# Kernel optimization log

Hardware: AMD Instinct MI355X
Metric: run time of the kernel (lower is better)

## Reference

```python
import jax, jax.numpy as jnp
import numpy as np

B, T, H, N = 2, 1024, 32, 64
HN = H * N              # 2048 hidden size
KVH, KVD = 8, 512       # GQA kv heads / kv width; repeat = HN // KVD = 4
LW, LA, LV, LG, LK = 64, 64, 32, 128, 32   # wavgk_split_list
EPS = 1e-6

def _rms(x, w):
    xf = x.astype(jnp.float32)
    var = jnp.mean(xf * xf, axis=-1, keepdims=True)
    return (w * (xf * jax.lax.rsqrt(var + EPS))).astype(x.dtype)

def _rot_half(x):
    x1, x2 = jnp.split(x, 2, axis=-1)
    return jnp.concatenate([-x2, x1], axis=-1)

def setup_inputs():
    key = jax.random.key(0)
    ks = iter(jax.random.split(key, 32))
    nrm = lambda s, sc=1.0: jax.random.normal(next(ks), s, jnp.float32) * sc
    d = {
        'x_in': nrm((B, T, HN)),
        'v_first': nrm((B, T, KVH, N)),
        'k_first': nrm((B, T, KVH, N)),
        'state': jnp.zeros((B, H, N, N), jnp.float32),
    }
    pos = jnp.arange(T, dtype=jnp.float32)
    inv = 1.0 / (10000.0 ** (jnp.arange(0, N, 2, dtype=jnp.float32) / N))
    ang = pos[:, None] * inv[None, :]
    ang = jnp.concatenate([ang, ang], axis=-1)   # [T, N]
    d['calc_cos'] = jnp.broadcast_to(jnp.cos(ang), (B, T, N))
    d['calc_sin'] = jnp.broadcast_to(jnp.sin(ang), (B, T, N))
    d.update(
        wavgk1=nrm((HN, LW + LA + LV + LG + LK), 0.02),
        w0=jnp.zeros((HN,), jnp.float32), w2=nrm((LW, HN), 0.02),
        a0=jnp.zeros((HN,), jnp.float32), a2=nrm((LA, HN), 0.02),
        v0=jnp.zeros((KVD,), jnp.float32), v2=nrm((LV, KVD), 0.02),
        g2=nrm((LG, HN), 0.02),
        k0=jnp.zeros((KVD,), jnp.float32), k2=nrm((LK, KVD), 0.02),
        r_k=nrm((H, N), 0.1),
        RKV_w=nrm((HN + 2 * KVD, HN), 0.02),
        O_w=nrm((HN, HN), 0.02),
        R_bias=jnp.zeros((HN,), jnp.float32),
        K_bias=jnp.zeros((KVD,), jnp.float32),
        V_bias=jnp.zeros((KVD,), jnp.float32),
        O_bias=jnp.zeros((HN,), jnp.float32),
        ln_r=jnp.ones((N,), jnp.float32),
        ln_k=jnp.ones((N,), jnp.float32),
        ln1=jnp.ones((HN,), jnp.float32),
    )
    return d

def reference(x_in, v_first, k_first, state, calc_cos, calc_sin, wavgk1, w0, w2,
              a0, a2, v0, v2, g2, k0, k2, r_k, RKV_w, O_w, R_bias, K_bias,
              V_bias, O_bias, ln_r, ln_k, ln1):
    rep = HN // KVD
    x = _rms(x_in, ln1)
    rkv = x @ RKV_w.T                                   # dense form of fpx_matmul
    r, k, v = jnp.split(rkv, [HN, HN + KVD], axis=-1)
    xw, xa, xv, xg, xk = jnp.split(x @ wavgk1, [LW, LW + LA, LW + LA + LV, LW + LA + LV + LG], axis=-1)
    r = r + R_bias; k = k + K_bias; v = v + V_bias
    r = _rms(r.reshape(B, T, H, N), ln_r)
    k = _rms(k.reshape(B, T, KVH, N), ln_k)
    cos, sin = calc_cos[:, :, None, :], calc_sin[:, :, None, :]   # unsqueeze_dim=2
    r = r * cos + _rot_half(r) * sin
    k = k * cos + _rot_half(k) * sin
    v = v.reshape(B, T, KVH, N)
    # layer_id > 0 path: gated residual toward layer-0 v/k
    gate_v = jax.nn.sigmoid(xv @ v2 + v0).reshape(B, T, KVH, N)
    v = v + (v_first - v) * gate_v
    gate_k = jax.nn.sigmoid(xk @ k2 + k0).reshape(B, T, KVH, N)
    k = k + (k_first - k) * gate_k
    w = jnp.tanh(xw) @ w2 + w0
    w = -jax.nn.softplus(-w) - 0.5
    # GQA repeat kv heads to H
    k = jnp.broadcast_to(k[:, :, :, None, :], (B, T, KVH, rep, N)).reshape(B, T, HN)
    v = jnp.broadcast_to(v[:, :, :, None, :], (B, T, KVH, rep, N)).reshape(B, T, HN)
    r = r.reshape(B, T, HN)
    a = jax.nn.sigmoid(xa @ a2 + a0)
    g = jax.nn.sigmoid(xg) @ g2
    kh = k.reshape(B, T, H, N)
    kk = (kh / jnp.maximum(jnp.linalg.norm(kh, axis=-1, keepdims=True), 1e-12)).reshape(B, T, HN)
    k = k * (1.0 - w + a)
    aa, bb = -kk, kk * a
    w = -jnp.exp(w.astype(jnp.float32))                 # log-decay (negative)
    # RWKV-7 recurrence: S <- S*diag(exp(w)) + (S a) b^T + v k^T ; o = S r
    hv = lambda t: jnp.moveaxis(t.reshape(B, T, H, N).astype(jnp.float32), 1, 0)
    def step(S, ts):
        r_t, w_t, k_t, v_t, a_t, b_t = ts               # each [B,H,N]
        sa = jnp.einsum('bhvk,bhk->bhv', S, a_t)
        S = S * jnp.exp(w_t)[:, :, None, :] + sa[..., None] * b_t[:, :, None, :] + v_t[..., None] * k_t[:, :, None, :]
        return S, jnp.einsum('bhvk,bhk->bhv', S, r_t)
    _, o = jax.lax.scan(step, state.astype(jnp.float32), (hv(r), hv(w), hv(k), hv(v), hv(aa), hv(bb)))
    xx = jnp.moveaxis(o, 0, 1).reshape(B, T, HN) * float(N) ** -0.5
    r_, k_, v_ = (t.reshape(B, T, H, N) for t in (r, k, v))
    bonus = (jnp.sum(r_ * k_ * r_k, axis=-1, keepdims=True) * v_).reshape(B, T, HN)
    xx = xx.astype(x_in.dtype) + bonus
    return x_in + (xx * g) @ O_w.T + O_bias
```

## Files before the change

### kernel.cpp

```cpp
#include <hip/hip_runtime.h>
#include <hip/hip_bf16.h>

#define B_ 2
#define T_ 1024
#define H_ 32
#define N_ 64
#define HN_ 2048
#define KVH_ 8
#define KVD_ 512
#define MTOK 2048
#define SMN 7168
#define KCAT 320
#define CH 64
#define NCH 16
#define NCHUNK 1024

typedef __bf16 bf16x8 __attribute__((ext_vector_type(8)));
typedef float f32x4 __attribute__((ext_vector_type(4)));
typedef float f32x2 __attribute__((ext_vector_type(2)));

__device__ __forceinline__ float sigmf(float x) { return 1.f / (1.f + expf(-x)); }

__global__ void f2b_kernel(const float* __restrict__ in, __hip_bfloat16* __restrict__ out, int n) {
    int i = blockIdx.x * 256 + threadIdx.x;
    if (i < n) out[i] = __float2bfloat16(in[i]);
}

__global__ void transpose_f2b_kernel(const float* __restrict__ in, __hip_bfloat16* __restrict__ out,
                                     int rows, int cols) {
    long i = (long)blockIdx.x * 256 + threadIdx.x;
    if (i >= (long)rows * cols) return;
    int c = (int)(i / rows), r = (int)(i % rows);
    out[i] = __float2bfloat16(in[(size_t)r * cols + c]);
}

__global__ void build_wcat_kernel(const float* __restrict__ w2, const float* __restrict__ a2,
                                  const float* __restrict__ v2, const float* __restrict__ g2,
                                  const float* __restrict__ k2, __hip_bfloat16* __restrict__ out) {
    long i = (long)blockIdx.x * 256 + threadIdx.x;
    if (i >= (long)SMN * KCAT) return;
    int j = (int)(i / KCAT), k = (int)(i % KCAT);
    float v = 0.f;
    if (j < 2048)      { if (k < 64)             v = w2[(size_t)k * 2048 + j]; }
    else if (j < 4096) { if (k >= 64 && k < 128)  v = a2[(size_t)(k - 64) * 2048 + (j - 2048)]; }
    else if (j < 4608) { if (k >= 128 && k < 160) v = v2[(size_t)(k - 128) * 512 + (j - 4096)]; }
    else if (j < 6656) { if (k >= 160 && k < 288) v = g2[(size_t)(k - 160) * 2048 + (j - 4608)]; }
    else               { if (k >= 288)            v = k2[(size_t)(k - 288) * 512 + (j - 6656)]; }
    out[i] = __float2bfloat16(v);
}

__global__ __launch_bounds__(256) void rmsnorm_kernel(const float* __restrict__ x,
                                                      const float* __restrict__ ln1,
                                                      __hip_bfloat16* __restrict__ out) {
    const int bt = blockIdx.x, tid = threadIdx.x;
    const float* row = x + (size_t)bt * HN_;
    float4 v0 = *(const float4*)(row + tid * 8);
    float4 v1 = *(const float4*)(row + tid * 8 + 4);
    float s = v0.x*v0.x + v0.y*v0.y + v0.z*v0.z + v0.w*v0.w
            + v1.x*v1.x + v1.y*v1.y + v1.z*v1.z + v1.w*v1.w;
    for (int m = 1; m < 64; m <<= 1) s += __shfl_xor(s, m);
    __shared__ float red[4];
    if ((tid & 63) == 0) red[tid >> 6] = s;
    __syncthreads();
    s = red[0] + red[1] + red[2] + red[3];
    float scale = rsqrtf(s * (1.f / HN_) + 1e-6f);
    float vals[8] = {v0.x, v0.y, v0.z, v0.w, v1.x, v1.y, v1.z, v1.w};
    #pragma unroll
    for (int j = 0; j < 8; ++j)
        out[(size_t)bt * HN_ + tid * 8 + j] = __float2bfloat16(vals[j] * scale * ln1[tid * 8 + j]);
}

__global__ void xwmod_kernel(const float* __restrict__ in, __hip_bfloat16* __restrict__ out) {
    long i = (long)blockIdx.x * 256 + threadIdx.x;
    if (i >= (long)MTOK * KCAT) return;
    int c = (int)(i % KCAT);
    float x = in[i];
    if (c < 64) x = tanhf(x);
    else if (c >= 160 && c < 288) x = sigmf(x);
    out[i] = __float2bfloat16(x);
}

__global__ __launch_bounds__(256) void gemm_bt(const __hip_bfloat16* __restrict__ A,
                                               const __hip_bfloat16* __restrict__ B,
                                               float* __restrict__ C, int M, int N, int K,
                                               const float* __restrict__ bias,
                                               const float* __restrict__ addend) {
    __shared__ __align__(16) __hip_bfloat16 As[64][40];
    __shared__ __align__(16) __hip_bfloat16 Bs[64][40];
    const int tid = threadIdx.x;
    const int wave = tid >> 6, lane = tid & 63;
    const int wr = (wave >> 1) * 32, wc = (wave & 1) * 32;
    const int brow = blockIdx.y << 6, bcol = blockIdx.x << 6;
    const int lrow = tid >> 2, lcol = (tid & 3) << 3;
    const int fr = lane & 15, ko = (lane >> 4) << 3;
    f32x4 acc[2][2] = {};
    for (int k0 = 0; k0 < K; k0 += 32) {
        uint4 av = *(const uint4*)(A + (size_t)(brow + lrow) * K + k0 + lcol);
        uint4 bv = *(const uint4*)(B + (size_t)(bcol + lrow) * K + k0 + lcol);
        *(uint4*)(&As[lrow][lcol]) = av;
        *(uint4*)(&Bs[lrow][lcol]) = bv;
        __syncthreads();
        bf16x8 af0 = *(const bf16x8*)(&As[wr + fr][ko]);
        bf16x8 af1 = *(const bf16x8*)(&As[wr + 16 + fr][ko]);
        bf16x8 bf0 = *(const bf16x8*)(&Bs[wc + fr][ko]);
        bf16x8 bf1 = *(const bf16x8*)(&Bs[wc + 16 + fr][ko]);
        acc[0][0] = __builtin_amdgcn_mfma_f32_16x16x32_bf16(af0, bf0, acc[0][0], 0, 0, 0);
        acc[0][1] = __builtin_amdgcn_mfma_f32_16x16x32_bf16(af0, bf1, acc[0][1], 0, 0, 0);
        acc[1][0] = __builtin_amdgcn_mfma_f32_16x16x32_bf16(af1, bf0, acc[1][0], 0, 0, 0);
        acc[1][1] = __builtin_amdgcn_mfma_f32_16x16x32_bf16(af1, bf1, acc[1][1], 0, 0, 0);
        __syncthreads();
    }
    const int cr = (lane >> 4) << 2, cc = lane & 15;
    #pragma unroll
    for (int i = 0; i < 2; ++i)
        #pragma unroll
        for (int j = 0; j < 2; ++j)
            #pragma unroll
            for (int r = 0; r < 4; ++r) {
                int row = brow + wr + i * 16 + cr + r;
                int col = bcol + wc + j * 16 + cc;
                float v = acc[i][j][r];
                if (bias) v += bias[col];
                if (addend) v += addend[(size_t)row * N + col];
                C[(size_t)row * N + col] = v;
            }
}

__global__ __launch_bounds__(256) void compose_kernel(
    const float* __restrict__ RKV, const float* __restrict__ SM,
    const float* __restrict__ v_first, const float* __restrict__ k_first,
    const float* __restrict__ cosd, const float* __restrict__ sind,
    const float* __restrict__ R_bias, const float* __restrict__ K_bias,
    const float* __restrict__ V_bias, const float* __restrict__ w0,
    const float* __restrict__ a0, const float* __restrict__ v0b,
    const float* __restrict__ k0b, const float* __restrict__ ln_r,
    const float* __restrict__ ln_k, const float* __restrict__ r_k,
    char* __restrict__ SC, __hip_bfloat16* __restrict__ VB, float* __restrict__ SB) {
    __shared__ __align__(16) float rbuf[HN_];
    __shared__ __align__(16) float kbuf[KVD_];
    __shared__ __align__(16) float vbuf[KVD_];
    __shared__ float knorms[KVH_];
    __shared__ float cosb[64], sinb[64];
    const int bt = blockIdx.x;
    const int b = bt >> 10, t = bt & 1023;
    const int tid = threadIdx.x;
    const float* rkvrow = RKV + (size_t)bt * 3072;
    const float* smrow = SM + (size_t)bt * SMN;

    if (tid < 64) {
        cosb[tid] = cosd[(size_t)bt * 64 + tid];
        sinb[tid] = sind[(size_t)bt * 64 + tid];
    }

    const int h = tid >> 3;
    const int off = (tid & 7) << 3;
    const int n0 = tid << 3;
    float rraw[8];
    {
        float4 x0 = *(const float4*)(rkvrow + n0);
        float4 x1 = *(const float4*)(rkvrow + n0 + 4);
        float4 b0 = *(const float4*)(R_bias + n0);
        float4 b1 = *(const float4*)(R_bias + n0 + 4);
        rraw[0] = x0.x + b0.x; rraw[1] = x0.y + b0.y; rraw[2] = x0.z + b0.z; rraw[3] = x0.w + b0.w;
        rraw[4] = x1.x + b1.x; rraw[5] = x1.y + b1.y; rraw[6] = x1.z + b1.z; rraw[7] = x1.w + b1.w;
    }
    float rss = 0.f;
    #pragma unroll
    for (int j = 0; j < 8; ++j) { rss += rraw[j] * rraw[j]; rbuf[n0 + j] = rraw[j]; }
    rss += __shfl_xor(rss, 1); rss += __shfl_xor(rss, 2); rss += __shfl_xor(rss, 4);
    float rscale = rsqrtf(rss * (1.f / 64.f) + 1e-6f);

    const int kvh = tid >> 5;
    const int ko2 = (tid & 31) << 1;
    const int kidx = kvh * 64 + ko2;
    float kraw0 = rkvrow[2048 + kidx] + K_bias[kidx];
    float kraw1 = rkvrow[2048 + kidx + 1] + K_bias[kidx + 1];
    float kss = kraw0 * kraw0 + kraw1 * kraw1;
    kss += __shfl_xor(kss, 1); kss += __shfl_xor(kss, 2); kss += __shfl_xor(kss, 4);
    kss += __shfl_xor(kss, 8); kss += __shfl_xor(kss, 16);
    float kscale = rsqrtf(kss * (1.f / 64.f) + 1e-6f);
    kbuf[kidx] = kraw0; kbuf[kidx + 1] = kraw1;

    {
        float va = rkvrow[2560 + kidx] + V_bias[kidx];
        float vb2 = rkvrow[2560 + kidx + 1] + V_bias[kidx + 1];
        float gv0 = sigmf(smrow[4096 + kidx] + v0b[kidx]);
        float gv1 = sigmf(smrow[4096 + kidx + 1] + v0b[kidx + 1]);
        vbuf[kidx] = va + (v_first[(size_t)bt * 512 + kidx] - va) * gv0;
        vbuf[kidx + 1] = vb2 + (v_first[(size_t)bt * 512 + kidx + 1] - vb2) * gv1;
    }
    __syncthreads();

    float rf[8];
    #pragma unroll
    for (int j = 0; j < 8; ++j) {
        int nn = off + j;
        int nn2 = (nn + 32) & 63;
        float val = rbuf[h * 64 + nn] * rscale * ln_r[nn];
        float oth = rbuf[h * 64 + nn2] * rscale * ln_r[nn2];
        float rot = (nn < 32) ? -oth : oth;
        rf[j] = val * cosb[nn] + rot * sinb[nn];
    }
    float kfv[2];
    #pragma unroll
    for (int j = 0; j < 2; ++j) {
        int nn = ko2 + j;
        int nn2 = (nn + 32) & 63;
        float val = kbuf[kvh * 64 + nn] * kscale * ln_k[nn];
        float oth = kbuf[kvh * 64 + nn2] * kscale * ln_k[nn2];
        float rot = (nn < 32) ? -oth : oth;
        float kr = val * cosb[nn] + rot * sinb[nn];
        float gk = sigmf(smrow[6656 + kvh * 64 + nn] + k0b[kvh * 64 + nn]);
        kfv[j] = kr + (k_first[(size_t)bt * 512 + kvh * 64 + nn] - kr) * gk;
    }
    __syncthreads();
    kbuf[kidx] = kfv[0]; kbuf[kidx + 1] = kfv[1];
    float kn = kfv[0] * kfv[0] + kfv[1] * kfv[1];
    kn += __shfl_xor(kn, 1); kn += __shfl_xor(kn, 2); kn += __shfl_xor(kn, 4);
    kn += __shfl_xor(kn, 8); kn += __shfl_xor(kn, 16);
    if ((tid & 31) == 0) knorms[kvh] = fmaxf(sqrtf(kn), 1e-12f);
    __syncthreads();

    const float knv = knorms[h >> 2];
    char* scb = SC + ((size_t)(b * H_ + h) * T_ + t) * 896;
    __hip_bfloat16* us = (__hip_bfloat16*)scb;
    float* df = (float*)(scb + 640);
    float4 w1a = *(const float4*)(smrow + n0);
    float4 w1b = *(const float4*)(smrow + n0 + 4);
    float4 ara = *(const float4*)(smrow + 2048 + n0);
    float4 arb = *(const float4*)(smrow + 2048 + n0 + 4);
    float w1arr[8] = {w1a.x, w1a.y, w1a.z, w1a.w, w1b.x, w1b.y, w1b.z, w1b.w};
    float aarr[8] = {ara.x, ara.y, ara.z, ara.w, arb.x, arb.y, arb.z, arb.w};
    float bsum = 0.f;
    #pragma unroll
    for (int j = 0; j < 8; ++j) {
        int nn = off + j, n = n0 + j;
        float w1 = w1arr[j] + w0[n];
        float w2v = -log1pf(expf(-w1)) - 0.5f;
        float av = sigmf(aarr[j] + a0[n]);
        float dec = expf(-expf(w2v));
        float kb = kbuf[(h >> 2) * 64 + nn];
        float vbv = vbuf[(h >> 2) * 64 + nn];
        float kkv = kb / knv;
        float ksc = kb * (1.f - w2v + av);
        us[nn]       = __float2bfloat16(rf[j]);
        us[64 + nn]  = __float2bfloat16(ksc);
        us[128 + nn] = __float2bfloat16(-kkv);
        us[192 + nn] = __float2bfloat16(kkv * av);
        us[256 + nn] = __float2bfloat16(vbv);
        df[nn] = dec;
        VB[(size_t)bt * HN_ + n] = __float2bfloat16(vbv);
        bsum += rf[j] * ksc * r_k[h * 64 + nn];
    }
    bsum += __shfl_xor(bsum, 1); bsum += __shfl_xor(bsum, 2); bsum += __shfl_xor(bsum, 4);
    if ((tid & 7) == 0) SB[bt * H_ + h] = bsum;
}

__global__ __launch_bounds__(64, 2) void scan_pass1(
    const char* __restrict__ SC, float* __restrict__ Q, float* __restrict__ O,
    float* __restrict__ Pf, float* __restrict__ Sf) {
    const int chunk = blockIdx.x;
    const int bh = chunk >> 4, c = chunk & 15;
    const int b = bh >> 5, h = bh & 31;
    const int lane = threadIdx.x;
    const char* base = SC + ((size_t)bh * T_ + (size_t)c * CH) * 896;

    f32x4 P4[16], S4[16];
    #pragma unroll
    for (int j = 0; j < 16; ++j) {
        #pragma unroll
        for (int e = 0; e < 4; ++e) {
            P4[j][e] = (4 * j + e == lane) ? 1.f : 0.f;
            S4[j][e] = 0.f;
        }
    }
    __shared__ __align__(16) float ld[2][5][64];
    float pr_r, pr_k, pr_a, pr_b, pr_v, pr_d;
    auto LOADT = [&](int t) {
        const __hip_bfloat16* us = (const __hip_bfloat16*)(base + (size_t)t * 896);
        pr_r = __bfloat162float(us[lane]);
        pr_k = __bfloat162float(us[64 + lane]);
        pr_a = __bfloat162float(us[128 + lane]);
        pr_b = __bfloat162float(us[192 + lane]);
        pr_v = __bfloat162float(us[256 + lane]);
        pr_d = *(const float*)(base + (size_t)t * 896 + 640 + 4 * lane);
    };
    LOADT(0);
    float* qbase = Q + (size_t)chunk * CH * 64 + lane;
    float* obase = O + ((size_t)b * T_ + (size_t)c * CH) * HN_ + h * 64 + lane;
    for (int t = 0; t < CH; ++t) {
        const int buf = t & 1;
        const float vt = pr_v;
        ld[buf][0][lane] = pr_a;
        ld[buf][1][lane] = pr_b;
        ld[buf][2][lane] = pr_d;
        ld[buf][3][lane] = pr_k;
        ld[buf][4][lane] = pr_r;
        __syncthreads();
        if (t + 1 < CH) LOADT(t + 1);
        f32x4 cp4 = {0,0,0,0}, sa4 = {0,0,0,0};
        #pragma unroll
        for (int j = 0; j < 16; ++j) {
            f32x4 a4 = *(const f32x4*)&ld[buf][0][4 * j];
            cp4 += P4[j] * a4;
            sa4 += S4[j] * a4;
        }
        const float cP = cp4[0] + cp4[1] + cp4[2] + cp4[3];
        const float sa = sa4[0] + sa4[1] + sa4[2] + sa4[3];
        const f32x4 cPv = {cP, cP, cP, cP}, sav = {sa, sa, sa, sa}, vtv = {vt, vt, vt, vt};
        f32x4 q4 = {0,0,0,0}, ol4 = {0,0,0,0};
        #pragma unroll
        for (int j = 0; j < 16; ++j) {
            f32x4 d4 = *(const f32x4*)&ld[buf][2][4 * j];
            f32x4 b4 = *(const f32x4*)&ld[buf][1][4 * j];
            f32x4 k4 = *(const f32x4*)&ld[buf][3][4 * j];
            f32x4 r4 = *(const f32x4*)&ld[buf][4][4 * j];
            f32x4 Pn = P4[j] * d4 + cPv * b4;
            f32x4 Sn = S4[j] * d4 + sav * b4 + vtv * k4;
            P4[j] = Pn; S4[j] = Sn;
            q4 += Pn * r4;
            ol4 += Sn * r4;
        }
        qbase[(size_t)t * 64] = q4[0] + q4[1] + q4[2] + q4[3];
        obase[(size_t)t * HN_] = ol4[0] + ol4[1] + ol4[2] + ol4[3];
        __syncthreads();
    }
    float* pf = Pf + (size_t)chunk * 4096 + lane * 64;
    float* sf = Sf + (size_t)chunk * 4096 + lane * 64;
    #pragma unroll
    for (int j = 0; j < 16; ++j) {
        *(f32x4*)(pf + 4 * j) = P4[j];
        *(f32x4*)(sf + 4 * j) = S4[j];
    }
}

__global__ __launch_bounds__(256) void scan_pass2(
    const float* __restrict__ Pf, float* __restrict__ Sf, const float* __restrict__ state) {
    const int blk = blockIdx.x;
    const int bh = blk >> 2, rb = blk & 3;
    const int tid = threadIdx.x;
    const int lv = tid >> 4, c0 = (tid & 15) << 2;
    __shared__ __align__(16) float S[16][68];
    __shared__ __align__(16) float P[64][64];

    *(f32x4*)&S[lv][c0] = *(const f32x4*)&state[(size_t)bh * 4096 + 1024 * rb + tid * 4];
    const size_t pbase = (size_t)(bh * NCH) * 4096;
    {
        f32x4 p0[4];
        #pragma unroll
        for (int j = 0; j < 4; ++j) p0[j] = *(const f32x4*)&Pf[pbase + tid * 16 + 4 * j];
        #pragma unroll
        for (int j = 0; j < 4; ++j) *(f32x4*)(&P[0][0] + tid * 16 + 4 * j) = p0[j];
    }
    __syncthreads();

    for (int c = 0; c < NCH; ++c) {
        const size_t ck = (size_t)(bh * NCH + c) * 4096;
        f32x4 pp[4];
        if (c + 1 < NCH) {
            #pragma unroll
            for (int j = 0; j < 4; ++j) pp[j] = *(const f32x4*)&Pf[ck + 4096 + tid * 16 + 4 * j];
        }
        f32x4 acc = *(const f32x4*)&Sf[ck + 1024 * rb + tid * 4];
        f32x4 cur = *(const f32x4*)&S[lv][c0];
        #pragma unroll 4
        for (int k4 = 0; k4 < 64; k4 += 4) {
            f32x4 sk4 = *(const f32x4*)&S[lv][k4];
            #pragma unroll
            for (int kk = 0; kk < 4; ++kk) {
                f32x4 pr = *(const f32x4*)&P[k4 + kk][c0];
                f32x4 sv = {sk4[kk], sk4[kk], sk4[kk], sk4[kk]};
                acc += sv * pr;
            }
        }
        __syncthreads();
        *(f32x4*)&S[lv][c0] = acc;
        if (c + 1 < NCH) {
            #pragma unroll
            for (int j = 0; j < 4; ++j) *(f32x4*)(&P[0][0] + tid * 16 + 4 * j) = pp[j];
        }
        *(f32x4*)&Sf[ck + 1024 * rb + tid * 4] = cur;
        __syncthreads();
    }
}

__global__ __launch_bounds__(64) void scan_pass3(
    const float* __restrict__ Q, const float* __restrict__ Sinit, float* __restrict__ O) {
    const int chunk = blockIdx.x;
    const int bh = chunk >> 4, c = chunk & 15;
    const int b = bh >> 5, h = bh & 31;
    const int t = threadIdx.x;
    __shared__ __align__(16) float S[64][64];
    #pragma unroll
    for (int j = 0; j < 16; ++j)
        *(f32x4*)&S[t][4 * j] = *(const f32x4*)&Sinit[(size_t)chunk * 4096 + (size_t)t * 64 + 4 * j];
    __syncthreads();
    float q[64];
    #pragma unroll
    for (int j = 0; j < 16; ++j)
        *(f32x4*)&q[4 * j] = *(const f32x4*)&Q[((size_t)chunk * CH + t) * 64 + 4 * j];
    float* orow = O + ((size_t)b * T_ + (size_t)c * CH + t) * HN_ + h * 64;
    #pragma unroll 4
    for (int v = 0; v < 64; ++v) {
        f32x4 a = {0, 0, 0, 0};
        #pragma unroll
        for (int j = 0; j < 16; ++j)
            a += *(const f32x4*)&S[v][4 * j] * *(const f32x4*)&q[4 * j];
        orow[v] = (a[0] + a[1] + a[2] + a[3] + orow[v]) * 0.125f;
    }
}

__global__ void post_kernel(const float* __restrict__ O, const float* __restrict__ SB,
                            const __hip_bfloat16* __restrict__ VB, const float* __restrict__ SM,
                            __hip_bfloat16* __restrict__ Ub) {
    long i = (long)blockIdx.x * 256 + threadIdx.x;
    if (i >= (long)MTOK * HN_) return;
    int bt = (int)(i >> 11), n = (int)(i & 2047), h = n >> 6;
    float u = (O[i] + SB[bt * H_ + h] * __bfloat162float(VB[i])) * SM[(size_t)bt * SMN + 4608 + n];
    Ub[i] = __float2bfloat16(u);
}

extern "C" void kernel_launch(void* const* d_in, const int* in_sizes, int n_in,
                              void* d_out, int out_size, void* d_ws, size_t ws_size,
                              hipStream_t stream) {
    (void)in_sizes; (void)n_in; (void)out_size; (void)ws_size;
    const float* x_in    = (const float*)d_in[0];
    const float* v_first = (const float*)d_in[1];
    const float* k_first = (const float*)d_in[2];
    const float* state   = (const float*)d_in[3];
    const float* calc_cos= (const float*)d_in[4];
    const float* calc_sin= (const float*)d_in[5];
    const float* wavgk1  = (const float*)d_in[6];
    const float* w0      = (const float*)d_in[7];
    const float* w2      = (const float*)d_in[8];
    const float* a0      = (const float*)d_in[9];
    const float* a2      = (const float*)d_in[10];
    const float* v0      = (const float*)d_in[11];
    const float* v2      = (const float*)d_in[12];
    const float* g2      = (const float*)d_in[13];
    const float* k0      = (const float*)d_in[14];
    const float* k2      = (const float*)d_in[15];
    const float* r_k     = (const float*)d_in[16];
    const float* RKV_w   = (const float*)d_in[17];
    const float* O_w     = (const float*)d_in[18];
    const float* R_bias  = (const float*)d_in[19];
    const float* K_bias  = (const float*)d_in[20];
    const float* V_bias  = (const float*)d_in[21];
    const float* O_bias  = (const float*)d_in[22];
    const float* ln_r    = (const float*)d_in[23];
    const float* ln_k    = (const float*)d_in[24];
    const float* ln1     = (const float*)d_in[25];
    float* out = (float*)d_out;

    char* ws = (char*)d_ws;
    size_t off = 0;
    auto alloc = [&](size_t bytes) -> char* {
        char* p = ws + off;
        off = (off + bytes + 255) & ~(size_t)255;
        return p;
    };
    float* SMf = (float*)alloc((size_t)MTOK * SMN * 4);
    char*  SCb = alloc((size_t)64 * T_ * 896);
    __hip_bfloat16* Ub = (__hip_bfloat16*)SCb;
    __hip_bfloat16* VBb = (__hip_bfloat16*)alloc((size_t)MTOK * HN_ * 2);
    float* SBf = (float*)alloc((size_t)MTOK * H_ * 4);
    float* Of  = (float*)alloc((size_t)MTOK * HN_ * 4);
    __hip_bfloat16* OWb = (__hip_bfloat16*)alloc((size_t)2048 * 2048 * 2);

    size_t ovl = off;
    __hip_bfloat16* Xb     = (__hip_bfloat16*)alloc((size_t)MTOK * HN_ * 2);
    __hip_bfloat16* RKVb   = (__hip_bfloat16*)alloc((size_t)3072 * 2048 * 2);
    __hip_bfloat16* WT1b   = (__hip_bfloat16*)alloc((size_t)320 * 2048 * 2);
    __hip_bfloat16* Wcatb  = (__hip_bfloat16*)alloc((size_t)SMN * KCAT * 2);
    __hip_bfloat16* XWmodb = (__hip_bfloat16*)alloc((size_t)MTOK * KCAT * 2);
    float* RKVf  = (float*)alloc((size_t)MTOK * 3072 * 4);
    float* XWraw = (float*)alloc((size_t)MTOK * KCAT * 4);
    off = ovl;
    float* Qf  = (float*)alloc((size_t)NCHUNK * CH * 64 * 4);
    float* Pff = (float*)alloc((size_t)NCHUNK * 4096 * 4);
    float* Sff = (float*)alloc((size_t)NCHUNK * 4096 * 4);

    f2b_kernel<<<(3072 * 2048 + 255) / 256, 256, 0, stream>>>(RKV_w, RKVb, 3072 * 2048);
    f2b_kernel<<<(2048 * 2048 + 255) / 256, 256, 0, stream>>>(O_w, OWb, 2048 * 2048);
    transpose_f2b_kernel<<<(320 * 2048 + 255) / 256, 256, 0, stream>>>(wavgk1, WT1b, 2048, 320);
    build_wcat_kernel<<<(SMN * KCAT + 255) / 256, 256, 0, stream>>>(w2, a2, v2, g2, k2, Wcatb);

    rmsnorm_kernel<<<MTOK, 256, 0, stream>>>(x_in, ln1, Xb);

    gemm_bt<<<dim3(3072 / 64, MTOK / 64), 256, 0, stream>>>(Xb, RKVb, RKVf, MTOK, 3072, 2048, nullptr, nullptr);
    gemm_bt<<<dim3(320 / 64, MTOK / 64), 256, 0, stream>>>(Xb, WT1b, XWraw, MTOK, 320, 2048, nullptr, nullptr);
    xwmod_kernel<<<(MTOK * KCAT + 255) / 256, 256, 0, stream>>>(XWraw, XWmodb);
    gemm_bt<<<dim3(SMN / 64, MTOK / 64), 256, 0, stream>>>(XWmodb, Wcatb, SMf, MTOK, SMN, KCAT, nullptr, nullptr);

    compose_kernel<<<MTOK, 256, 0, stream>>>(RKVf, SMf, v_first, k_first, calc_cos, calc_sin,
                                             R_bias, K_bias, V_bias, w0, a0, v0, k0,
                                             ln_r, ln_k, r_k, SCb, VBb, SBf);

    scan_pass1<<<NCHUNK, 64, 0, stream>>>(SCb, Qf, Of, Pff, Sff);
    scan_pass2<<<B_ * H_ * 4, 256, 0, stream>>>(Pff, Sff, state);
    scan_pass3<<<NCHUNK, 64, 0, stream>>>(Qf, Sff, Of);

    post_kernel<<<(MTOK * HN_ + 255) / 256, 256, 0, stream>>>(Of, SBf, VBb, SMf, Ub);
    gemm_bt<<<dim3(HN_ / 64, MTOK / 64), 256, 0, stream>>>(Ub, OWb, out, MTOK, HN_, 2048, O_bias, x_in);
}
```

Measured before the change: 452.9 us.

## Add 128x128 MFMA GEMM tile and split scan pass1 across two waves

Adds a 128x128-tile bf16 MFMA GEMM, with a 64x64 tile per wave, and uses it for the RKV, SM and output projections. This raises data reuse per global load and cuts the number of blocks. Separately, scan_pass1 now runs two waves per chunk: one wave evolves the P matrix and writes Q, the other evolves S and writes O. This halves the per-thread register state and serial work. The larger GEMM tiles lower occupancy and leave fewer blocks to fill the CUs, for example 24x16 blocks on the RKV GEMM.

After: 462.4 us. 2.1% more time.

```diff
diff --git a/kernel.cpp b/kernel.cpp
--- a/kernel.cpp
+++ b/kernel.cpp
@@ -124,6 +124,63 @@
                 if (addend) v += addend[(size_t)row * N + col];
                 C[(size_t)row * N + col] = v;
             }
+}
+
+__global__ __launch_bounds__(256) void gemm_bt128(const __hip_bfloat16* __restrict__ A,
+                                                  const __hip_bfloat16* __restrict__ B,
+                                                  float* __restrict__ C, int M, int N, int K,
+                                                  const float* __restrict__ bias,
+                                                  const float* __restrict__ addend) {
+    __shared__ __align__(16) __hip_bfloat16 As[128][40];
+    __shared__ __align__(16) __hip_bfloat16 Bs[128][40];
+    const int tid = threadIdx.x;
+    const int wave = tid >> 6, lane = tid & 63;
+    const int wr = (wave >> 1) * 64, wc = (wave & 1) * 64;
+    const int brow = blockIdx.y << 7, bcol = blockIdx.x << 7;
+    const int lrow = tid >> 2, lcol = (tid & 3) << 3;
+    const int fr = lane & 15, ko = (lane >> 4) << 3;
+    f32x4 acc[4][4] = {};
+    const __hip_bfloat16* Ap = A + (size_t)(brow + lrow) * K + lcol;
+    const __hip_bfloat16* Bp = B + (size_t)(bcol + lrow) * K + lcol;
+    const size_t half = (size_t)64 * K;
+    for (int k0 = 0; k0 < K; k0 += 32) {
+        uint4 a0 = *(const uint4*)(Ap + k0);
+        uint4 a1 = *(const uint4*)(Ap + half + k0);
+        uint4 b0 = *(const uint4*)(Bp + k0);
+        uint4 b1 = *(const uint4*)(Bp + half + k0);
+        *(uint4*)(&As[lrow][lcol]) = a0;
+        *(uint4*)(&As[lrow + 64][lcol]) = a1;
+        *(uint4*)(&Bs[lrow][lcol]) = b0;
+        *(uint4*)(&Bs[lrow + 64][lcol]) = b1;
+        __syncthreads();
+        bf16x8 af[4], bfr[4];
+        #pragma unroll
+        for (int i = 0; i < 4; ++i) {
+            af[i]  = *(const bf16x8*)(&As[wr + i * 16 + fr][ko]);
+            bfr[i] = *(const bf16x8*)(&Bs[wc + i * 16 + fr][ko]);
+        }
+        #pragma unroll
+        for (int i = 0; i < 4; ++i)
+            #pragma unroll
+            for (int j = 0; j < 4; ++j)
+                acc[i][j] = __builtin_amdgcn_mfma_f32_16x16x32_bf16(af[i], bfr[j], acc[i][j], 0, 0, 0);
+        __syncthreads();
+    }
+    const int cr = (lane >> 4) << 2, cc = lane & 15;
+    #pragma unroll
+    for (int i = 0; i < 4; ++i)
+        #pragma unroll
+        for (int j = 0; j < 4; ++j) {
+            const int row0 = brow + wr + i * 16 + cr;
+            const int col = bcol + wc + j * 16 + cc;
+            #pragma unroll
+            for (int r = 0; r < 4; ++r) {
+                float v = acc[i][j][r];
+                if (bias) v += bias[col];
+                if (addend) v += addend[(size_t)(row0 + r) * N + col];
+                C[(size_t)(row0 + r) * N + col] = v;
+            }
+        }
 }
 
 __global__ __launch_bounds__(256) void compose_kernel(
@@ -256,82 +313,102 @@
     if ((tid & 7) == 0) SB[bt * H_ + h] = bsum;
 }
 
-__global__ __launch_bounds__(64, 2) void scan_pass1(
+__global__ __launch_bounds__(128) void scan_pass1(
     const char* __restrict__ SC, float* __restrict__ Q, float* __restrict__ O,
     float* __restrict__ Pf, float* __restrict__ Sf) {
     const int chunk = blockIdx.x;
     const int bh = chunk >> 4, c = chunk & 15;
     const int b = bh >> 5, h = bh & 31;
-    const int lane = threadIdx.x;
+    const int tid = threadIdx.x;
+    const int wid = tid >> 6, lane = tid & 63;
     const char* base = SC + ((size_t)bh * T_ + (size_t)c * CH) * 896;
-
-    f32x4 P4[16], S4[16];
-    #pragma unroll
-    for (int j = 0; j < 16; ++j) {
-        #pragma unroll
-        for (int e = 0; e < 4; ++e) {
-            P4[j][e] = (4 * j + e == lane) ? 1.f : 0.f;
-            S4[j][e] = 0.f;
-        }
-    }
     __shared__ __align__(16) float ld[2][5][64];
-    float pr_r, pr_k, pr_a, pr_b, pr_v, pr_d;
+
+    f32x4 R4[16];
+    #pragma unroll
+    for (int j = 0; j < 16; ++j)
+        #pragma unroll
+        for (int e = 0; e < 4; ++e)
+            R4[j][e] = (wid == 0 && 4 * j + e == lane) ? 1.f : 0.f;
+
+    float p0, p1, p2;
     auto LOADT = [&](int t) {
         const __hip_bfloat16* us = (const __hip_bfloat16*)(base + (size_t)t * 896);
-        pr_r = __bfloat162float(us[lane]);
-        pr_k = __bfloat162float(us[64 + lane]);
-        pr_a = __bfloat162float(us[128 + lane]);
-        pr_b = __bfloat162float(us[192 + lane]);
-        pr_v = __bfloat162float(us[256 + lane]);
-        pr_d = *(const float*)(base + (size_t)t * 896 + 640 + 4 * lane);
+        if (wid == 0) {
+            p0 = __bfloat162float(us[128 + lane]);
+            p1 = __bfloat162float(us[192 + lane]);
+            p2 = __bfloat162float(us[lane]);
+        } else {
+            p0 = *(const float*)(base + (size_t)t * 896 + 640 + 4 * lane);
+            p1 = __bfloat162float(us[64 + lane]);
+            p2 = __bfloat162float(us[256 + lane]);
+        }
     };
     LOADT(0);
     float* qbase = Q + (size_t)chunk * CH * 64 + lane;
     float* obase = O + ((size_t)b * T_ + (size_t)c * CH) * HN_ + h * 64 + lane;
     for (int t = 0; t < CH; ++t) {
         const int buf = t & 1;
-        const float vt = pr_v;
-        ld[buf][0][lane] = pr_a;
-        ld[buf][1][lane] = pr_b;
-        ld[buf][2][lane] = pr_d;
-        ld[buf][3][lane] = pr_k;
-        ld[buf][4][lane] = pr_r;
+        float vt = 0.f;
+        if (wid == 0) {
+            ld[buf][0][lane] = p0;
+            ld[buf][1][lane] = p1;
+            ld[buf][4][lane] = p2;
+        } else {
+            ld[buf][2][lane] = p0;
+            ld[buf][3][lane] = p1;
+            vt = p2;
+        }
         __syncthreads();
         if (t + 1 < CH) LOADT(t + 1);
-        f32x4 cp4 = {0,0,0,0}, sa4 = {0,0,0,0};
-        #pragma unroll
-        for (int j = 0; j < 16; ++j) {
-            f32x4 a4 = *(const f32x4*)&ld[buf][0][4 * j];
-            cp4 += P4[j] * a4;
-            sa4 += S4[j] * a4;
-        }
-        const float cP = cp4[0] + cp4[1] + cp4[2] + cp4[3];
-        const float sa = sa4[0] + sa4[1] + sa4[2] + sa4[3];
-        const f32x4 cPv = {cP, cP, cP, cP}, sav = {sa, sa, sa, sa}, vtv = {vt, vt, vt, vt};
-        f32x4 q4 = {0,0,0,0}, ol4 = {0,0,0,0};
-        #pragma unroll
-        for (int j = 0; j < 16; ++j) {
-            f32x4 d4 = *(const f32x4*)&ld[buf][2][4 * j];
-            f32x4 b4 = *(const f32x4*)&ld[buf][1][4 * j];
-            f32x4 k4 = *(const f32x4*)&ld[buf][3][4 * j];
-            f32x4 r4 = *(const f32x4*)&ld[buf][4][4 * j];
-            f32x4 Pn = P4[j] * d4 + cPv * b4;
-            f32x4 Sn = S4[j] * d4 + sav * b4 + vtv * k4;
-            P4[j] = Pn; S4[j] = Sn;
-            q4 += Pn * r4;
-            ol4 += Sn * r4;
-        }
-        qbase[(size_t)t * 64] = q4[0] + q4[1] + q4[2] + q4[3];
-        obase[(size_t)t * HN_] = ol4[0] + ol4[1] + ol4[2] + ol4[3];
-        __syncthreads();
-    }
-    float* pf = Pf + (size_t)chunk * 4096 + lane * 64;
-    float* sf = Sf + (size_t)chunk * 4096 + lane * 64;
-    #pragma unroll
-    for (int j = 0; j < 16; ++j) {
-        *(f32x4*)(pf + 4 * j) = P4[j];
-        *(f32x4*)(sf + 4 * j) = S4[j];
-    }
+        f32x4 da = {0,0,0,0}, db = {0,0,0,0};
+        #pragma unroll
+        for (int j = 0; j < 16; j += 2) {
+            da += R4[j]     * *(const f32x4*)&ld[buf][0][4 * j];
+            db += R4[j + 1] * *(const f32x4*)&ld[buf][0][4 * j + 4];
+        }
+        const float dot = da[0] + da[1] + da[2] + da[3] + db[0] + db[1] + db[2] + db[3];
+        const f32x4 dotv = {dot, dot, dot, dot};
+        f32x4 qa = {0,0,0,0}, qb = {0,0,0,0};
+        if (wid == 0) {
+            #pragma unroll
+            for (int j = 0; j < 16; j += 2) {
+                f32x4 d0 = *(const f32x4*)&ld[buf][2][4 * j];
+                f32x4 b0 = *(const f32x4*)&ld[buf][1][4 * j];
+                f32x4 r0 = *(const f32x4*)&ld[buf][4][4 * j];
+                f32x4 Pn = R4[j] * d0 + dotv * b0;
+                R4[j] = Pn; qa += Pn * r0;
+                f32x4 d1 = *(const f32x4*)&ld[buf][2][4 * j + 4];
+                f32x4 b1 = *(const f32x4*)&ld[buf][1][4 * j + 4];
+                f32x4 r1 = *(const f32x4*)&ld[buf][4][4 * j + 4];
+                f32x4 Pm = R4[j + 1] * d1 + dotv * b1;
+                R4[j + 1] = Pm; qb += Pm * r1;
+            }
+            qbase[(size_t)t * 64] = qa[0]+qa[1]+qa[2]+qa[3]+qb[0]+qb[1]+qb[2]+qb[3];
+        } else {
+            const f32x4 vtv = {vt, vt, vt, vt};
+            #pragma unroll
+            for (int j = 0; j < 16; j += 2) {
+                f32x4 d0 = *(const f32x4*)&ld[buf][2][4 * j];
+                f32x4 b0 = *(const f32x4*)&ld[buf][1][4 * j];
+                f32x4 k0 = *(const f32x4*)&ld[buf][3][4 * j];
+                f32x4 r0 = *(const f32x4*)&ld[buf][4][4 * j];
+                f32x4 Sn = R4[j] * d0 + dotv * b0 + vtv * k0;
+                R4[j] = Sn; qa += Sn * r0;
+                f32x4 d1 = *(const f32x4*)&ld[buf][2][4 * j + 4];
+                f32x4 b1 = *(const f32x4*)&ld[buf][1][4 * j + 4];
+                f32x4 k1 = *(const f32x4*)&ld[buf][3][4 * j + 4];
+                f32x4 r1 = *(const f32x4*)&ld[buf][4][4 * j + 4];
+                f32x4 Sm = R4[j + 1] * d1 + dotv * b1 + vtv * k1;
+                R4[j + 1] = Sm; qb += Sm * r1;
+            }
+            obase[(size_t)t * HN_] = qa[0]+qa[1]+qa[2]+qa[3]+qb[0]+qb[1]+qb[2]+qb[3];
+        }
+    }
+    float* fp = (wid == 0 ? Pf : Sf) + (size_t)chunk * 4096 + lane * 64;
+    #pragma unroll
+    for (int j = 0; j < 16; ++j)
+        *(f32x4*)(fp + 4 * j) = R4[j];
 }
 
 __global__ __launch_bounds__(256) void scan_pass2(
@@ -487,19 +564,19 @@
 
     rmsnorm_kernel<<<MTOK, 256, 0, stream>>>(x_in, ln1, Xb);
 
-    gemm_bt<<<dim3(3072 / 64, MTOK / 64), 256, 0, stream>>>(Xb, RKVb, RKVf, MTOK, 3072, 2048, nullptr, nullptr);
+    gemm_bt128<<<dim3(3072 / 128, MTOK / 128), 256, 0, stream>>>(Xb, RKVb, RKVf, MTOK, 3072, 2048, nullptr, nullptr);
     gemm_bt<<<dim3(320 / 64, MTOK / 64), 256, 0, stream>>>(Xb, WT1b, XWraw, MTOK, 320, 2048, nullptr, nullptr);
     xwmod_kernel<<<(MTOK * KCAT + 255) / 256, 256, 0, stream>>>(XWraw, XWmodb);
-    gemm_bt<<<dim3(SMN / 64, MTOK / 64), 256, 0, stream>>>(XWmodb, Wcatb, SMf, MTOK, SMN, KCAT, nullptr, nullptr);
+    gemm_bt128<<<dim3(SMN / 128, MTOK / 128), 256, 0, stream>>>(XWmodb, Wcatb, SMf, MTOK, SMN, KCAT, nullptr, nullptr);
 
     compose_kernel<<<MTOK, 256, 0, stream>>>(RKVf, SMf, v_first, k_first, calc_cos, calc_sin,
                                              R_bias, K_bias, V_bias, w0, a0, v0, k0,
                                              ln_r, ln_k, r_k, SCb, VBb, SBf);
 
-    scan_pass1<<<NCHUNK, 64, 0, stream>>>(SCb, Qf, Of, Pff, Sff);
+    scan_pass1<<<NCHUNK, 128, 0, stream>>>(SCb, Qf, Of, Pff, Sff);
     scan_pass2<<<B_ * H_ * 4, 256, 0, stream>>>(Pff, Sff, state);
     scan_pass3<<<NCHUNK, 64, 0, stream>>>(Qf, Sff, Of);
 
     post_kernel<<<(MTOK * HN_ + 255) / 256, 256, 0, stream>>>(Of, SBf, VBb, SMf, Ub);
-    gemm_bt<<<dim3(HN_ / 64, MTOK / 64), 256, 0, stream>>>(Ub, OWb, out, MTOK, HN_, 2048, O_bias, x_in);
-}
+    gemm_bt128<<<dim3(HN_ / 128, MTOK / 128), 256, 0, stream>>>(Ub, OWb, out, MTOK, HN_, 2048, O_bias, x_in);
+}
```
